# Kernel tuning notes

Hardware: AMD Instinct MI355X
Metric: run time of the kernel (lower is better)

The kernel has to match this reference:

```python
import jax, jax.numpy as jnp
import numpy as np

B, S, D, H, DH = 4, 2048, 1024, 16, 64

def setup_inputs() -> dict:
    key = jax.random.key(0)
    ks = jax.random.split(key, 8)
    scale = 1.0 / np.sqrt(D)  # mimic lecun_normal-ish scaling
    return {
        "inputs_q": jax.random.normal(ks[0], (B, S, D), jnp.float32),
        "inputs_kv": jax.random.normal(ks[1], (B, S, D), jnp.float32),
        "Wq": jax.random.normal(ks[2], (D, H, DH), jnp.float32) * scale,
        "bq": jnp.zeros((H, DH), jnp.float32),
        "Wk": jax.random.normal(ks[3], (D, H, DH), jnp.float32) * scale,
        "bk": jnp.zeros((H, DH), jnp.float32),
        "Wv": jax.random.normal(ks[4], (D, H, DH), jnp.float32) * scale,
        "bv": jnp.zeros((H, DH), jnp.float32),
        "Wo": jax.random.normal(ks[5], (H, DH, D), jnp.float32) * (1.0 / np.sqrt(H * DH)),
        "bo": jnp.zeros((D,), jnp.float32),
    }

def reference(inputs_q, inputs_kv, Wq, bq, Wk, bk, Wv, bv, Wo, bo):
    # QKV projections: [B,S,D] x [D,H,Dh] -> [B,S,H,Dh]
    q = jnp.einsum('bsd,dhf->bshf', inputs_q, Wq) + bq
    k = jnp.einsum('bsd,dhf->bshf', inputs_kv, Wk) + bk
    v = jnp.einsum('bsd,dhf->bshf', inputs_kv, Wv) + bv
    q = q / jnp.sqrt(jnp.asarray(DH, q.dtype))
    # attention scores [B,H,Sq,Sk]
    scores = jnp.einsum('bqhf,bkhf->bhqk', q, k)
    probs = jax.nn.softmax(scores, axis=-1)
    x = jnp.einsum('bhqk,bkhf->bqhf', probs, v)
    # output projection over (H, Dh)
    out = jnp.einsum('bqhf,hfd->bqd', x, Wo) + bo
    return out
```

## Files before the change

kernel.cpp:

```cpp
#include <hip/hip_runtime.h>
#include <hip/hip_bf16.h>
#include <hip/hip_fp16.h>
#include <math.h>

#define B_   4
#define S_   2048
#define D_   1024
#define H_   16
#define DH_  64
#define M_   (B_ * S_)
#define N_   (H_ * DH_)

typedef _Float16 f16;
typedef __attribute__((ext_vector_type(2))) _Float16 f16x2;
typedef __attribute__((ext_vector_type(4))) _Float16 f16x4;
typedef __attribute__((ext_vector_type(8))) _Float16 f16x8;
typedef __attribute__((ext_vector_type(4))) float    f32x4;

union H8 { f16x8 v; f16x4 q[2]; f16x2 d[4]; };
union PK { __half2 h2; f16x2 v; };

#if __has_builtin(__builtin_amdgcn_exp2f)
__device__ __forceinline__ float exp2_fast(float x) { return __builtin_amdgcn_exp2f(x); }
#else
__device__ __forceinline__ float exp2_fast(float x) {
  float r; asm("v_exp_f32 %0, %1" : "=v"(r) : "v"(x)); return r;
}
#endif

__device__ __forceinline__ void async_cp16(const void* g, void* l) {
  __builtin_amdgcn_global_load_lds(
      (const __attribute__((address_space(1))) unsigned int*)g,
      (__attribute__((address_space(3))) unsigned int*)l, 16, 0, 0);
}

__global__ __launch_bounds__(256) void cvt_f32_f16(const float* __restrict__ in,
                                                   f16* __restrict__ out, int n4) {
  int i = blockIdx.x * 256 + threadIdx.x;
  if (i < n4) {
    f32x4 v = ((const f32x4*)in)[i];
    ((f16x4*)out)[i] = __builtin_convertvector(v, f16x4);
  }
}

__global__ __launch_bounds__(256) void transpose_w(
    const float* __restrict__ W0, const float* __restrict__ W1,
    const float* __restrict__ W2, const float* __restrict__ W3,
    f16* __restrict__ T0, f16* __restrict__ T1,
    f16* __restrict__ T2, f16* __restrict__ T3) {
  const float* W = (blockIdx.z == 0) ? W0 : (blockIdx.z == 1) ? W1
                 : (blockIdx.z == 2) ? W2 : W3;
  f16* T = (blockIdx.z == 0) ? T0 : (blockIdx.z == 1) ? T1
         : (blockIdx.z == 2) ? T2 : T3;
  __shared__ float tile[32][33];
  int x  = blockIdx.x * 32 + threadIdx.x;
  int y0 = blockIdx.y * 32 + threadIdx.y;
#pragma unroll
  for (int i = 0; i < 32; i += 8)
    tile[threadIdx.y + i][threadIdx.x] = W[(size_t)(y0 + i) * 1024 + x];
  __syncthreads();
  int tx  = blockIdx.y * 32 + threadIdx.x;
  int ty0 = blockIdx.x * 32 + threadIdx.y;
#pragma unroll
  for (int i = 0; i < 32; i += 8)
    T[(size_t)(ty0 + i) * 1024 + tx] = (f16)tile[threadIdx.x][threadIdx.y + i];
}

__global__ __launch_bounds__(256) void transpose_v(const f16* __restrict__ v,
                                                   f16* __restrict__ vt) {
  int bh = blockIdx.y;
  int b  = bh >> 4, h = bh & 15;
  int s0 = blockIdx.x * 64;
  __shared__ f16 tile[64][72];
  int tid = threadIdx.x;
#pragma unroll
  for (int it = 0; it < 16; ++it) {
    int idx = it * 256 + tid;
    int r = idx >> 6, c = idx & 63;
    tile[r][c] = v[((size_t)(b * S_ + s0 + r)) * N_ + h * DH_ + c];
  }
  __syncthreads();
#pragma unroll
  for (int it = 0; it < 16; ++it) {
    int idx = it * 256 + tid;
    int fr = idx >> 6, sc = idx & 63;
    vt[((size_t)bh * DH_ + fr) * S_ + s0 + sc] = tile[sc][fr];
  }
}

template <bool OUT_F32>
__global__ __launch_bounds__(256) void gemm_bt(
    const f16* __restrict__ A, const f16* __restrict__ Bt,
    const float* __restrict__ bias, float scale,
    void* __restrict__ outp, int M, int N, int K) {
  __shared__ f16 lA[128 * 64];
  __shared__ f16 lB[128 * 64];
  const int nbx = N >> 7;
  const int cpx = gridDim.x >> 3;
  const int wg  = (blockIdx.x & 7) * cpx + (blockIdx.x >> 3);
  const int tile_m = (wg / nbx) * 128, tile_n = (wg % nbx) * 128;
  const int tid  = threadIdx.x;
  const int lane = tid & 63, wid = tid >> 6;
  const int wr = wid >> 1, wc = wid & 1;
  const int l8 = lane >> 3, c8 = (lane & 7) * 8;
  const int r15 = lane & 15, hi = lane >> 4;

  f32x4 acc[4][4];
#pragma unroll
  for (int m = 0; m < 4; ++m)
#pragma unroll
    for (int n = 0; n < 4; ++n) acc[m][n] = (f32x4)(0.f);

  for (int kt = 0; kt < K; kt += 64) {
#pragma unroll
    for (int i = 0; i < 4; ++i) {
      int rb = wid * 32 + i * 8;
      async_cp16(A  + (size_t)(tile_m + rb + l8) * K + kt + c8, &lA[rb * 64]);
      async_cp16(Bt + (size_t)(tile_n + rb + l8) * K + kt + c8, &lB[rb * 64]);
    }
    __syncthreads();
#pragma unroll
    for (int kk = 0; kk < 2; ++kk) {
      f16x8 af[4], bf[4];
#pragma unroll
      for (int m = 0; m < 4; ++m)
        af[m] = *(const f16x8*)&lA[(wr * 64 + m * 16 + r15) * 64 + kk * 32 + hi * 8];
#pragma unroll
      for (int n = 0; n < 4; ++n)
        bf[n] = *(const f16x8*)&lB[(wc * 64 + n * 16 + r15) * 64 + kk * 32 + hi * 8];
#pragma unroll
      for (int m = 0; m < 4; ++m)
#pragma unroll
        for (int n = 0; n < 4; ++n)
          acc[m][n] = __builtin_amdgcn_mfma_f32_16x16x32_f16(af[m], bf[n], acc[m][n], 0, 0, 0);
    }
    __syncthreads();
  }

#pragma unroll
  for (int m = 0; m < 4; ++m) {
    int row0 = tile_m + wr * 64 + m * 16 + hi * 4;
#pragma unroll
    for (int n = 0; n < 4; ++n) {
      int col = tile_n + wc * 64 + n * 16 + r15;
      float bv = bias[col];
#pragma unroll
      for (int r = 0; r < 4; ++r) {
        float v = (acc[m][n][r] + bv) * scale;
        if (OUT_F32)
          ((float*)outp)[(size_t)(row0 + r) * N + col] = v;
        else
          ((f16*)outp)[(size_t)(row0 + r) * N + col] = (f16)v;
      }
    }
  }
}

__global__ __launch_bounds__(256, 2) void attn(
    const f16* __restrict__ q, const f16* __restrict__ k,
    const f16* __restrict__ vt, f16* __restrict__ x) {
  __shared__ f16 lK[2][64 * 64];
  __shared__ f16 lV[2][64 * 64];
  const int tid = threadIdx.x, lane = tid & 63, wid = tid >> 6;
  const int bh = blockIdx.y, b = bh >> 4, h = bh & 15;
  const int q0 = blockIdx.x * 256 + wid * 64;
  const int c15 = lane & 15, hi = lane >> 4;
  const int swr = (c15 & 7) << 4;
  const int swz = 8 * ((lane & 7) ^ (lane >> 3));
  const int lrow = lane >> 3;

  const f16* qb = q  + (size_t)b * S_ * N_ + h * DH_;
  const f16* kb = k  + (size_t)b * S_ * N_ + h * DH_;
  const f16* vb = vt + (size_t)bh * DH_ * S_;

  f16x8 qf[4][2];
#pragma unroll
  for (int qm = 0; qm < 4; ++qm)
#pragma unroll
    for (int kk = 0; kk < 2; ++kk)
      qf[qm][kk] = *(const f16x8*)(qb + (size_t)(q0 + qm * 16 + c15) * N_ + kk * 32 + hi * 8);

  f32x4 xa[4][4];
#pragma unroll
  for (int fn = 0; fn < 4; ++fn)
#pragma unroll
    for (int qm = 0; qm < 4; ++qm) xa[fn][qm] = (f32x4)(0.f);
  float rm[4], rl[4];
#pragma unroll
  for (int qm = 0; qm < 4; ++qm) { rm[qm] = -INFINITY; rl[qm] = 0.f; }

  auto STAGE = [&](int t, int buf) {
    int j0 = t * 64;
#pragma unroll
    for (int i = 0; i < 2; ++i) {
      int rb = wid * 16 + i * 8;
      async_cp16(kb + (size_t)(j0 + rb + lrow) * N_ + swz, &lK[buf][rb * 64]);
      async_cp16(vb + (size_t)(rb + lrow) * S_ + j0 + swz, &lV[buf][rb * 64]);
    }
  };

  STAGE(0, 0);
  __syncthreads();

  for (int t = 0; t < S_ / 64; ++t) {
    const int cur = t & 1;
    if (t < S_ / 64 - 1) STAGE(t + 1, cur ^ 1);

    f16x8 kf[4][2];
#pragma unroll
    for (int jn = 0; jn < 4; ++jn) {
      int rowe = (jn * 16 + c15) * 64;
#pragma unroll
      for (int kk = 0; kk < 2; ++kk)
        kf[jn][kk] = *(const f16x8*)&lK[cur][rowe + (((kk * 64 + hi * 16) ^ swr) >> 1)];
    }

    f16x8 bfrag[4][2];
#pragma unroll
    for (int qm = 0; qm < 4; ++qm) {
      f32x4 sq[4];
#pragma unroll
      for (int jn = 0; jn < 4; ++jn) sq[jn] = (f32x4)(0.f);
#pragma unroll
      for (int kk = 0; kk < 2; ++kk)
#pragma unroll
        for (int jn = 0; jn < 4; ++jn)
          sq[jn] = __builtin_amdgcn_mfma_f32_16x16x32_f16(kf[jn][kk], qf[qm][kk], sq[jn], 0, 0, 0);

      float mx = sq[0][0];
#pragma unroll
      for (int jn = 0; jn < 4; ++jn)
#pragma unroll
        for (int r = 0; r < 4; ++r) mx = fmaxf(mx, sq[jn][r]);
      mx = fmaxf(mx, __shfl_xor(mx, 16));
      mx = fmaxf(mx, __shfl_xor(mx, 32));
      float nm  = fmaxf(rm[qm], mx);
      float fac = exp2_fast(rm[qm] - nm);
      rm[qm] = nm;

      float p[4][4], ts = 0.f;
#pragma unroll
      for (int jn = 0; jn < 4; ++jn)
#pragma unroll
        for (int r = 0; r < 4; ++r) {
          p[jn][r] = exp2_fast(sq[jn][r] - nm);
          ts += p[jn][r];
        }
      ts += __shfl_xor(ts, 16);
      ts += __shfl_xor(ts, 32);
      rl[qm] = rl[qm] * fac + ts;
#pragma unroll
      for (int fn = 0; fn < 4; ++fn)
#pragma unroll
        for (int r = 0; r < 4; ++r) xa[fn][qm][r] *= fac;

      PK w[4][2];
#pragma unroll
      for (int jn = 0; jn < 4; ++jn)
#pragma unroll
        for (int hh = 0; hh < 2; ++hh)
          w[jn][hh].h2 = __floats2half2_rn(p[jn][2 * hh], p[jn][2 * hh + 1]);
#pragma unroll
      for (int kk = 0; kk < 2; ++kk) {
        H8 u;
        u.d[0] = w[2 * kk][0].v;     u.d[1] = w[2 * kk][1].v;
        u.d[2] = w[2 * kk + 1][0].v; u.d[3] = w[2 * kk + 1][1].v;
        bfrag[qm][kk] = u.v;
      }
    }

#pragma unroll
    for (int kk = 0; kk < 2; ++kk)
#pragma unroll
      for (int fn = 0; fn < 4; ++fn) {
        int rowe = (fn * 16 + c15) * 64;
        H8 u;
        u.q[0] = *(const f16x4*)&lV[cur][rowe + (((kk * 64 + hi * 8) ^ swr) >> 1)];
        u.q[1] = *(const f16x4*)&lV[cur][rowe + (((kk * 64 + 32 + hi * 8) ^ swr) >> 1)];
#pragma unroll
        for (int qm = 0; qm < 4; ++qm)
          xa[fn][qm] = __builtin_amdgcn_mfma_f32_16x16x32_f16(u.v, bfrag[qm][kk], xa[fn][qm], 0, 0, 0);
      }
    __syncthreads();
  }

  float inv[4];
#pragma unroll
  for (int qm = 0; qm < 4; ++qm) inv[qm] = 1.f / rl[qm];
#pragma unroll
  for (int qm = 0; qm < 4; ++qm) {
    size_t rowb = (size_t)(b * S_ + q0 + qm * 16 + c15) * N_ + h * DH_;
#pragma unroll
    for (int fn = 0; fn < 4; ++fn) {
      f16x4 o;
#pragma unroll
      for (int r = 0; r < 4; ++r) o[r] = (f16)(xa[fn][qm][r] * inv[qm]);
      *(f16x4*)(x + rowb + fn * 16 + hi * 4) = o;
    }
  }
}

extern "C" void kernel_launch(void* const* d_in, const int* in_sizes, int n_in,
                              void* d_out, int out_size, void* d_ws, size_t ws_size,
                              hipStream_t stream) {
  const float* inq  = (const float*)d_in[0];
  const float* inkv = (const float*)d_in[1];
  const float* Wq = (const float*)d_in[2];
  const float* bq = (const float*)d_in[3];
  const float* Wk = (const float*)d_in[4];
  const float* bk = (const float*)d_in[5];
  const float* Wv = (const float*)d_in[6];
  const float* bv = (const float*)d_in[7];
  const float* Wo = (const float*)d_in[8];
  const float* bo = (const float*)d_in[9];
  float* out = (float*)d_out;

  char* ws = (char*)d_ws;
  const size_t MB = 1024 * 1024;
  f16* h_inq  = (f16*)(ws + 0);
  f16* h_inkv = (f16*)(ws + 16 * MB);
  f16* h_WqT  = (f16*)(ws + 32 * MB);
  f16* h_WkT  = (f16*)(ws + 34 * MB);
  f16* h_WvT  = (f16*)(ws + 36 * MB);
  f16* h_WoT  = (f16*)(ws + 38 * MB);
  f16* h_q    = (f16*)(ws + 40 * MB);
  f16* h_k    = (f16*)(ws + 56 * MB);
  f16* h_v    = (f16*)(ws + 72 * MB);
  f16* h_vt   = h_inq;
  f16* h_x    = h_inkv;

  const int nIn = M_ * D_;
  cvt_f32_f16<<<nIn / 4 / 256, 256, 0, stream>>>(inq,  h_inq,  nIn / 4);
  cvt_f32_f16<<<nIn / 4 / 256, 256, 0, stream>>>(inkv, h_inkv, nIn / 4);
  transpose_w<<<dim3(32, 32, 4), dim3(32, 8), 0, stream>>>(
      Wq, Wk, Wv, Wo, h_WqT, h_WkT, h_WvT, h_WoT);
  const float qscale = 0.125f * 1.4426950408889634f;
  const int nwg = (M_ / 128) * (N_ / 128);
  gemm_bt<false><<<nwg, 256, 0, stream>>>(h_inq,  h_WqT, bq, qscale, h_q, M_, N_, D_);
  gemm_bt<false><<<nwg, 256, 0, stream>>>(h_inkv, h_WkT, bk, 1.0f,   h_k, M_, N_, D_);
  gemm_bt<false><<<nwg, 256, 0, stream>>>(h_inkv, h_WvT, bv, 1.0f,   h_v, M_, N_, D_);
  transpose_v<<<dim3(S_ / 64, B_ * H_), 256, 0, stream>>>(h_v, h_vt);
  attn<<<dim3(S_ / 256, B_ * H_), 256, 0, stream>>>(h_q, h_k, h_vt, h_x);
  gemm_bt<true><<<nwg, 256, 0, stream>>>(h_x, h_WoT, bo, 1.0f, out, M_, D_, N_);
}
```

Baseline: 366.3 us.

## Fuse QKV GEMMs, double-buffer GEMM LDS, lazy softmax rescale, MFMA priority

Merges the three QKV projection GEMMs into one launch and adds double-buffered LDS staging to both GEMMs, so global loads for the next K tile overlap MFMA work. In attention, the online-softmax rescale of accumulators is skipped whenever the new max exceeds the running max by at most 8 (log2 units), and s_setprio is raised around the MFMA blocks. The lazy rescale lets probabilities exceed 1 before f16 packing, which costs some precision margin. Double buffering doubles LDS use per GEMM block, which may reduce occupancy.

Result: no change. 373.0 us (+1.8%).

```diff
diff --git a/kernel.cpp b/kernel.cpp
--- a/kernel.cpp
+++ b/kernel.cpp
@@ -88,13 +88,91 @@
   }
 }
 
-template <bool OUT_F32>
-__global__ __launch_bounds__(256) void gemm_bt(
+__global__ __launch_bounds__(256) void gemm_qkv(
+    const f16* __restrict__ Aq, const f16* __restrict__ Akv,
+    const f16* __restrict__ WqT, const f16* __restrict__ WkT, const f16* __restrict__ WvT,
+    const float* __restrict__ bq, const float* __restrict__ bk, const float* __restrict__ bv,
+    float qscale, f16* __restrict__ oq, f16* __restrict__ ok, f16* __restrict__ ov) {
+  __shared__ f16 lA[2][128 * 64];
+  __shared__ f16 lB[2][128 * 64];
+  const int cpx = gridDim.x >> 3;
+  const int wg  = (blockIdx.x & 7) * cpx + (blockIdx.x >> 3);
+  const int tile_m = (wg / 24) * 128;
+  const int nt = wg % 24, part = nt >> 3;
+  const int tile_n = (nt & 7) * 128;
+  const f16* A  = (part == 0) ? Aq : Akv;
+  const f16* Bt = ((part == 0) ? WqT : (part == 1) ? WkT : WvT) + (size_t)tile_n * D_;
+  const float* bias = ((part == 0) ? bq : (part == 1) ? bk : bv) + tile_n;
+  f16* outp = ((part == 0) ? oq : (part == 1) ? ok : ov);
+  const float scale = (part == 0) ? qscale : 1.0f;
+
+  const int tid  = threadIdx.x;
+  const int lane = tid & 63, wid = tid >> 6;
+  const int wr = wid >> 1, wc = wid & 1;
+  const int l8 = lane >> 3, c8 = (lane & 7) * 8;
+  const int r15 = lane & 15, hi = lane >> 4;
+
+  f32x4 acc[4][4];
+#pragma unroll
+  for (int m = 0; m < 4; ++m)
+#pragma unroll
+    for (int n = 0; n < 4; ++n) acc[m][n] = (f32x4)(0.f);
+
+  auto STAGE = [&](int t, int buf) {
+    int kt = t * 64;
+#pragma unroll
+    for (int i = 0; i < 4; ++i) {
+      int rb = wid * 32 + i * 8;
+      async_cp16(A  + (size_t)(tile_m + rb + l8) * D_ + kt + c8, &lA[buf][rb * 64]);
+      async_cp16(Bt + (size_t)(rb + l8) * D_ + kt + c8, &lB[buf][rb * 64]);
+    }
+  };
+
+  STAGE(0, 0);
+  __syncthreads();
+  for (int t = 0; t < D_ / 64; ++t) {
+    const int cur = t & 1;
+    if (t + 1 < D_ / 64) STAGE(t + 1, cur ^ 1);
+#pragma unroll
+    for (int kk = 0; kk < 2; ++kk) {
+      f16x8 af[4], bf[4];
+#pragma unroll
+      for (int m = 0; m < 4; ++m)
+        af[m] = *(const f16x8*)&lA[cur][(wr * 64 + m * 16 + r15) * 64 + kk * 32 + hi * 8];
+#pragma unroll
+      for (int n = 0; n < 4; ++n)
+        bf[n] = *(const f16x8*)&lB[cur][(wc * 64 + n * 16 + r15) * 64 + kk * 32 + hi * 8];
+#pragma unroll
+      for (int m = 0; m < 4; ++m)
+#pragma unroll
+        for (int n = 0; n < 4; ++n)
+          acc[m][n] = __builtin_amdgcn_mfma_f32_16x16x32_f16(af[m], bf[n], acc[m][n], 0, 0, 0);
+    }
+    __syncthreads();
+  }
+
+#pragma unroll
+  for (int m = 0; m < 4; ++m) {
+    int row0 = tile_m + wr * 64 + m * 16 + hi * 4;
+#pragma unroll
+    for (int n = 0; n < 4; ++n) {
+      int col = wc * 64 + n * 16 + r15;
+      float bv_ = bias[col];
+#pragma unroll
+      for (int r = 0; r < 4; ++r) {
+        float v = (acc[m][n][r] + bv_) * scale;
+        outp[(size_t)(row0 + r) * N_ + tile_n + col] = (f16)v;
+      }
+    }
+  }
+}
+
+__global__ __launch_bounds__(256) void gemm_out(
     const f16* __restrict__ A, const f16* __restrict__ Bt,
-    const float* __restrict__ bias, float scale,
-    void* __restrict__ outp, int M, int N, int K) {
-  __shared__ f16 lA[128 * 64];
-  __shared__ f16 lB[128 * 64];
+    const float* __restrict__ bias, float* __restrict__ outp,
+    int M, int N, int K) {
+  __shared__ f16 lA[2][128 * 64];
+  __shared__ f16 lB[2][128 * 64];
   const int nbx = N >> 7;
   const int cpx = gridDim.x >> 3;
   const int wg  = (blockIdx.x & 7) * cpx + (blockIdx.x >> 3);
@@ -111,23 +189,31 @@
 #pragma unroll
     for (int n = 0; n < 4; ++n) acc[m][n] = (f32x4)(0.f);
 
-  for (int kt = 0; kt < K; kt += 64) {
+  auto STAGE = [&](int t, int buf) {
+    int kt = t * 64;
 #pragma unroll
     for (int i = 0; i < 4; ++i) {
       int rb = wid * 32 + i * 8;
-      async_cp16(A  + (size_t)(tile_m + rb + l8) * K + kt + c8, &lA[rb * 64]);
-      async_cp16(Bt + (size_t)(tile_n + rb + l8) * K + kt + c8, &lB[rb * 64]);
-    }
-    __syncthreads();
+      async_cp16(A  + (size_t)(tile_m + rb + l8) * K + kt + c8, &lA[buf][rb * 64]);
+      async_cp16(Bt + (size_t)(tile_n + rb + l8) * K + kt + c8, &lB[buf][rb * 64]);
+    }
+  };
+
+  STAGE(0, 0);
+  __syncthreads();
+  const int T = K / 64;
+  for (int t = 0; t < T; ++t) {
+    const int cur = t & 1;
+    if (t + 1 < T) STAGE(t + 1, cur ^ 1);
 #pragma unroll
     for (int kk = 0; kk < 2; ++kk) {
       f16x8 af[4], bf[4];
 #pragma unroll
       for (int m = 0; m < 4; ++m)
-        af[m] = *(const f16x8*)&lA[(wr * 64 + m * 16 + r15) * 64 + kk * 32 + hi * 8];
+        af[m] = *(const f16x8*)&lA[cur][(wr * 64 + m * 16 + r15) * 64 + kk * 32 + hi * 8];
 #pragma unroll
       for (int n = 0; n < 4; ++n)
-        bf[n] = *(const f16x8*)&lB[(wc * 64 + n * 16 + r15) * 64 + kk * 32 + hi * 8];
+        bf[n] = *(const f16x8*)&lB[cur][(wc * 64 + n * 16 + r15) * 64 + kk * 32 + hi * 8];
 #pragma unroll
       for (int m = 0; m < 4; ++m)
 #pragma unroll
@@ -145,13 +231,8 @@
       int col = tile_n + wc * 64 + n * 16 + r15;
       float bv = bias[col];
 #pragma unroll
-      for (int r = 0; r < 4; ++r) {
-        float v = (acc[m][n][r] + bv) * scale;
-        if (OUT_F32)
-          ((float*)outp)[(size_t)(row0 + r) * N + col] = v;
-        else
-          ((f16*)outp)[(size_t)(row0 + r) * N + col] = (f16)v;
-      }
+      for (int r = 0; r < 4; ++r)
+        outp[(size_t)(row0 + r) * N + col] = acc[m][n][r] + bv;
     }
   }
 }
@@ -221,11 +302,13 @@
       f32x4 sq[4];
 #pragma unroll
       for (int jn = 0; jn < 4; ++jn) sq[jn] = (f32x4)(0.f);
+      __builtin_amdgcn_s_setprio(1);
 #pragma unroll
       for (int kk = 0; kk < 2; ++kk)
 #pragma unroll
         for (int jn = 0; jn < 4; ++jn)
           sq[jn] = __builtin_amdgcn_mfma_f32_16x16x32_f16(kf[jn][kk], qf[qm][kk], sq[jn], 0, 0, 0);
+      __builtin_amdgcn_s_setprio(0);
 
       float mx = sq[0][0];
 #pragma unroll
@@ -234,25 +317,38 @@
         for (int r = 0; r < 4; ++r) mx = fmaxf(mx, sq[jn][r]);
       mx = fmaxf(mx, __shfl_xor(mx, 16));
       mx = fmaxf(mx, __shfl_xor(mx, 32));
-      float nm  = fmaxf(rm[qm], mx);
-      float fac = exp2_fast(rm[qm] - nm);
-      rm[qm] = nm;
 
       float p[4][4], ts = 0.f;
-#pragma unroll
-      for (int jn = 0; jn < 4; ++jn)
-#pragma unroll
-        for (int r = 0; r < 4; ++r) {
-          p[jn][r] = exp2_fast(sq[jn][r] - nm);
-          ts += p[jn][r];
-        }
-      ts += __shfl_xor(ts, 16);
-      ts += __shfl_xor(ts, 32);
-      rl[qm] = rl[qm] * fac + ts;
-#pragma unroll
-      for (int fn = 0; fn < 4; ++fn)
-#pragma unroll
-        for (int r = 0; r < 4; ++r) xa[fn][qm][r] *= fac;
+      if (__all(mx - rm[qm] <= 8.0f)) {
+#pragma unroll
+        for (int jn = 0; jn < 4; ++jn)
+#pragma unroll
+          for (int r = 0; r < 4; ++r) {
+            p[jn][r] = exp2_fast(sq[jn][r] - rm[qm]);
+            ts += p[jn][r];
+          }
+        ts += __shfl_xor(ts, 16);
+        ts += __shfl_xor(ts, 32);
+        rl[qm] += ts;
+      } else {
+        float nm  = fmaxf(rm[qm], mx);
+        float fac = exp2_fast(rm[qm] - nm);
+        rm[qm] = nm;
+#pragma unroll
+        for (int jn = 0; jn < 4; ++jn)
+#pragma unroll
+          for (int r = 0; r < 4; ++r) {
+            p[jn][r] = exp2_fast(sq[jn][r] - nm);
+            ts += p[jn][r];
+          }
+        ts += __shfl_xor(ts, 16);
+        ts += __shfl_xor(ts, 32);
+        rl[qm] = rl[qm] * fac + ts;
+#pragma unroll
+        for (int fn = 0; fn < 4; ++fn)
+#pragma unroll
+          for (int r = 0; r < 4; ++r) xa[fn][qm][r] *= fac;
+      }
 
       PK w[4][2];
 #pragma unroll
@@ -269,6 +365,7 @@
       }
     }
 
+    __builtin_amdgcn_s_setprio(1);
 #pragma unroll
     for (int kk = 0; kk < 2; ++kk)
 #pragma unroll
@@ -281,6 +378,7 @@
         for (int qm = 0; qm < 4; ++qm)
           xa[fn][qm] = __builtin_amdgcn_mfma_f32_16x16x32_f16(u.v, bfrag[qm][kk], xa[fn][qm], 0, 0, 0);
       }
+    __builtin_amdgcn_s_setprio(0);
     __syncthreads();
   }
 
@@ -335,11 +433,9 @@
   transpose_w<<<dim3(32, 32, 4), dim3(32, 8), 0, stream>>>(
       Wq, Wk, Wv, Wo, h_WqT, h_WkT, h_WvT, h_WoT);
   const float qscale = 0.125f * 1.4426950408889634f;
-  const int nwg = (M_ / 128) * (N_ / 128);
-  gemm_bt<false><<<nwg, 256, 0, stream>>>(h_inq,  h_WqT, bq, qscale, h_q, M_, N_, D_);
-  gemm_bt<false><<<nwg, 256, 0, stream>>>(h_inkv, h_WkT, bk, 1.0f,   h_k, M_, N_, D_);
-  gemm_bt<false><<<nwg, 256, 0, stream>>>(h_inkv, h_WvT, bv, 1.0f,   h_v, M_, N_, D_);
+  gemm_qkv<<<1536, 256, 0, stream>>>(h_inq, h_inkv, h_WqT, h_WkT, h_WvT,
+                                     bq, bk, bv, qscale, h_q, h_k, h_v);
   transpose_v<<<dim3(S_ / 64, B_ * H_), 256, 0, stream>>>(h_v, h_vt);
   attn<<<dim3(S_ / 256, B_ * H_), 256, 0, stream>>>(h_q, h_k, h_vt, h_x);
-  gemm_bt<true><<<nwg, 256, 0, stream>>>(h_x, h_WoT, bo, 1.0f, out, M_, D_, N_);
-}
+  gemm_out<<<(M_ / 128) * (N_ / 128), 256, 0, stream>>>(h_x, h_WoT, bo, out, M_, N_, D_);
+}
```
